# Performance work log

Hardware: AMD Instinct MI355X
Metric: run time of the kernel (lower is better)

The kernel has to match this reference:

```python
import jax, jax.numpy as jnp
import numpy as np

D_MODEL = 256
N_FEATURES = 32768
N_BLOCKS = 8
MIN_FEATURES = 512
BATCH = 2048
ALPHA = 0.99          # RunningAvgNormalizer alpha
EPS_CTRL = 3e-4       # L1RegController eps
TARGET_L0 = 100.0


def _pareto_seg(n_features, n_blocks, min_features, rng):
    # mirrors get_pareto_block_bounds, returning per-feature block ids
    cdf = 1.0 - (np.arange(n_features - min_features + 1) / (n_features - min_features + 1)) ** 0.5
    pdf = np.concatenate([np.zeros(min_features), np.abs(cdf[1:] - cdf[:-1])])
    pdf = pdf / pdf.sum()
    sp = np.sort(rng.choice(n_features, size=n_blocks - 1, replace=False, p=pdf))
    return np.searchsorted(sp, np.arange(n_features), side='right').astype(np.int32)


def setup_inputs() -> dict:
    key = jax.random.key(0)
    k0, k1 = jax.random.split(key, 2)
    x = jax.random.normal(k0, (BATCH, D_MODEL), jnp.float32)
    W_enc = jax.random.normal(k1, (D_MODEL, N_FEATURES), jnp.float32) / np.sqrt(D_MODEL)
    b_enc = -0.04 * jnp.ones((N_FEATURES,), jnp.float32)
    W_dec = (0.1 * W_enc / jnp.linalg.norm(W_enc, axis=0, keepdims=True)).T
    b_dec = jnp.zeros((D_MODEL,), jnp.float32)
    bw = np.arange(1, N_BLOCKS + 1, dtype=np.float32) ** 1.0  # block_weight_power = 1.0
    block_weights = jnp.asarray(bw / bw.max())
    running_avg = jnp.asarray([np.sqrt(D_MODEL)], jnp.float32)  # warmed-up running norm
    l1_scale = jnp.ones((1,), jnp.float32)
    seg = jnp.asarray(_pareto_seg(N_FEATURES, N_BLOCKS, MIN_FEATURES, np.random.default_rng(0)))
    return {"x": x, "W_enc": W_enc, "b_enc": b_enc, "W_dec": W_dec, "b_dec": b_dec,
            "block_weights": block_weights, "running_avg": running_avg,
            "l1_scale": l1_scale, "seg": seg}


def reference(x, W_enc, b_enc, W_dec, b_dec, block_weights, running_avg, l1_scale, seg):
    K = block_weights.shape[0]
    B, d = x.shape
    # RunningAvgNormalizer.normalize(update=True): update EMA, then scale (no grad through EMA)
    ra = ALPHA * running_avg[0] + (1.0 - ALPHA) * jnp.mean(jnp.linalg.norm(x, axis=-1))
    ra = jax.lax.stop_gradient(ra)
    xn = x * (jnp.sqrt(jnp.float32(d)) / ra)
    acts = jax.nn.relu(xn @ W_enc + b_enc)                       # [B, F]
    Wd_norms = jnp.linalg.norm(W_dec, axis=1)                    # [F]
    # per-block log-loss: sum over block features of mean-over-batch log term
    per_feat = jnp.mean(jnp.log(acts * Wd_norms + 0.1) - jnp.log(0.1), axis=0)  # [F]
    block_l1 = jax.ops.segment_sum(per_feat, seg, num_segments=K)               # [K]
    l1_loss = jnp.mean(block_weights * jnp.cumsum(block_l1))
    # per-block decode: (acts masked to block) @ W_dec, sequential over K small blocks
    onehot = (seg[None, :] == jnp.arange(K)[:, None]).astype(acts.dtype)  # [K, F]
    block_preds = jax.lax.map(lambda m: (acts * m) @ W_dec, onehot)       # [K, B, d]
    cum_preds = jnp.cumsum(block_preds, axis=0) + b_dec                   # b_dec added to preds[0] pre-cumsum
    block_errs = jnp.mean(jnp.sum((cum_preds - xn[None]) ** 2, axis=-1), axis=-1) * block_weights
    mse_loss = jnp.mean(block_errs)
    # L1RegController (no-grad)
    avg_l0 = jax.lax.stop_gradient(jnp.sum(acts > 0).astype(jnp.float32) / B)
    l1_reg_scale = jnp.where(avg_l0 < TARGET_L0, l1_scale[0] * (1.0 - EPS_CTRL), l1_scale[0] * (1.0 + EPS_CTRL))
    loss = mse_loss + l1_reg_scale * l1_loss
    return loss
```

## Files before the change

### kernel.cpp

```cpp
#include <hip/hip_runtime.h>
#include <hip/hip_fp8.h>

typedef float  f32x4  __attribute__((ext_vector_type(4)));
typedef unsigned short u16;
typedef unsigned int   u32;
typedef unsigned long long u64;

#define BATCH 2048
#define DM    256
#define NFEAT 32768
#define NBLK  8
#define ALPHA_C   0.99f
#define EPS_CTRL  3e-4f
#define TARGET_L0 100.0f

#define BT    32
#define FC    2048
#define NCHUNK (NFEAT / FC)
#define MACRO 128
#define NMACRO (FC / MACRO)
#define NPMAX 24
#define ACTS_SZ (BT * MACRO)

#define SCL_WE 8.0f
#define INV_WE 0.125f
#define SCL_WD 16.0f
#define INV_WD 0.0625f

#define WS_RA    0
#define WS_SCALE 1
#define WS_L0    2
#define WS_L1    4
#define WS_ERR   16
#define WSI_BND  32
#define WSI_PTN  40
#define WSI_PTS  41
#define WSI_PSEG 66
#define WS_WDN   256
#define PIECES_OFF_BYTES ((size_t)262144)
#define PIECES_BYTES ((size_t)NPMAX * BATCH * DM * 2)
#define WEP_OFF_BYTES (PIECES_OFF_BYTES + PIECES_BYTES)
#define WDP_OFF_BYTES (WEP_OFF_BYTES + (size_t)NFEAT * DM)

#define RAW_BARRIER() asm volatile("s_waitcnt lgkmcnt(0)\n\ts_barrier" ::: "memory")

static __device__ inline u16 f2b(float f) {
    return __builtin_bit_cast(u16, (__bf16)f);
}
static __device__ inline float b2f(u16 u) {
    return (float)__builtin_bit_cast(__bf16, u);
}
static __device__ inline u32 f2f8x2(float a, float b) {
#if __has_builtin(__builtin_amdgcn_cvt_pk_fp8_f32)
    return ((u32)__builtin_amdgcn_cvt_pk_fp8_f32(a, b, 0, false)) & 0xFFFFu;
#else
    __hip_fp8_e4m3 ha(a), hb(b);
    return (u32)(*reinterpret_cast<unsigned char*>(&ha)) |
           ((u32)(*reinterpret_cast<unsigned char*>(&hb)) << 8);
#endif
}
static __device__ inline f32x4 mfma8(u64 a, u64 b, f32x4 c) {
    return __builtin_amdgcn_mfma_f32_16x16x32_fp8_fp8((long)a, (long)b, c, 0, 0, 0);
}

__global__ __launch_bounds__(256) void k_prep(const float* __restrict__ x,
                                              const int* __restrict__ seg,
                                              float* ws) {
    const int bid = blockIdx.x;
    const int wave = threadIdx.x >> 6, lane = threadIdx.x & 63;
    if (bid < BATCH / 4) {
        const int row = bid * 4 + wave;
        const float4 v = *reinterpret_cast<const float4*>(x + (size_t)row * DM + lane * 4);
        float s = v.x * v.x + v.y * v.y + v.z * v.z + v.w * v.w;
        #pragma unroll
        for (int o = 32; o; o >>= 1) s += __shfl_xor(s, o);
        if (lane == 0) atomicAdd(&ws[WS_RA], sqrtf(s));
    } else {
        const int f = (bid - BATCH / 4) * 256 + threadIdx.x;
        if (f > 0 && f < NFEAT) {
            const int s = seg[f];
            if (s != seg[f - 1]) ((int*)ws)[WSI_BND + s] = f;
        }
    }
}

__global__ void k_pt2(const int* __restrict__ seg,
                      const float* __restrict__ ravg, float* ws) {
    __shared__ int stv[NCHUNK + NBLK];
    __shared__ int outL[NPMAX];
    __shared__ int NL;
    int* wsi = (int*)ws;
    const int t = threadIdx.x;
    if (t < NCHUNK) stv[t] = t * FC;
    else if (t < NCHUNK + NBLK - 1) stv[t] = wsi[WSI_BND + (t - NCHUNK + 1)];
    __syncthreads();
    if (t == 0) {
        int i = 0, j = NCHUNK, N = 0;
        while (i < NCHUNK || j < NCHUNK + NBLK - 1) {
            int v;
            if (i < NCHUNK && (j >= NCHUNK + NBLK - 1 || stv[i] <= stv[j])) v = stv[i++];
            else v = stv[j++];
            if (N == 0 || outL[N - 1] != v) outL[N++] = v;
        }
        NL = N;
    }
    __syncthreads();
    const int N = NL;
    if (t < N) {
        wsi[WSI_PTS + t] = outL[t];
        wsi[WSI_PSEG + t] = seg[outL[t]];
    }
    if (t == 0) {
        wsi[WSI_PTN] = N;
        wsi[WSI_PTS + N] = NFEAT;
        float ra = ALPHA_C * ravg[0] + (1.0f - ALPHA_C) * (ws[WS_RA] / (float)BATCH);
        ws[WS_SCALE] = 16.0f / ra;
    }
}

__global__ __launch_bounds__(256) void k_pack(const float* __restrict__ We,
                                              const float* __restrict__ Wd,
                                              unsigned char* __restrict__ WeP,
                                              unsigned char* __restrict__ WdP,
                                              float* ws) {
    __shared__ float tile[32][261];
    const int t = threadIdx.x;
    const int bid = blockIdx.x;
    if (bid < 1024) {
        const int kf = bid & 7, fblk = bid >> 3;
        const int f0 = fblk * 256;
        #pragma unroll
        for (int p = 0; p < 8; ++p) {
            const int r = p * 4 + (t >> 6);
            const int c = (t & 63) * 4;
            const float4 v = *reinterpret_cast<const float4*>(We + (size_t)(kf * 32 + r) * NFEAT + f0 + c);
            tile[r][c] = v.x; tile[r][c + 1] = v.y; tile[r][c + 2] = v.z; tile[r][c + 3] = v.w;
        }
        __syncthreads();
        #pragma unroll
        for (int p = 0; p < 4; ++p) {
            const int item = p * 256 + t;
            const int g = item >> 6, l = item & 63;
            const int F = fblk * 16 + g;
            float tv[8];
            #pragma unroll
            for (int i = 0; i < 8; ++i)
                tv[i] = tile[(l >> 4) * 8 + i][g * 16 + (l & 15)] * SCL_WE;
            const u32 lo = f2f8x2(tv[0], tv[1]) | (f2f8x2(tv[2], tv[3]) << 16);
            const u32 hi = f2f8x2(tv[4], tv[5]) | (f2f8x2(tv[6], tv[7]) << 16);
            *reinterpret_cast<u64*>(WeP + ((size_t)(F * 8 + kf) * 64 + l) * 8) = (u64)lo | ((u64)hi << 32);
        }
    } else {
        const int G = bid - 1024;
        #pragma unroll
        for (int p = 0; p < 8; ++p) {
            const int r = p * 4 + (t >> 6);
            const int c = (t & 63) * 4;
            const float4 v = *reinterpret_cast<const float4*>(Wd + (size_t)(G * 32 + r) * DM + c);
            tile[r][c] = v.x; tile[r][c + 1] = v.y; tile[r][c + 2] = v.z; tile[r][c + 3] = v.w;
        }
        __syncthreads();
        {
            const int row = t >> 3, part = t & 7;
            float s = 0.0f;
            #pragma unroll
            for (int j = 0; j < 32; ++j) {
                const float xv = tile[row][part * 32 + j];
                s += xv * xv;
            }
            s += __shfl_xor(s, 1); s += __shfl_xor(s, 2); s += __shfl_xor(s, 4);
            if (part == 0) ws[WS_WDN + G * 32 + row] = sqrtf(s);
        }
        #pragma unroll
        for (int p = 0; p < 4; ++p) {
            const int item = p * 256 + t;
            const int g = item >> 6, l = item & 63;
            float tv[8];
            #pragma unroll
            for (int i = 0; i < 8; ++i)
                tv[i] = tile[(l >> 4) * 8 + i][g * 16 + (l & 15)] * SCL_WD;
            const u32 lo = f2f8x2(tv[0], tv[1]) | (f2f8x2(tv[2], tv[3]) << 16);
            const u32 hi = f2f8x2(tv[4], tv[5]) | (f2f8x2(tv[6], tv[7]) << 16);
            *reinterpret_cast<u64*>(WdP + ((size_t)(g * 1024 + G) * 64 + l) * 8) = (u64)lo | ((u64)hi << 32);
        }
    }
}

__global__ __launch_bounds__(256, 2) void k_main(const float* __restrict__ x,
                                                 const float* __restrict__ be,
                                                 const int* __restrict__ seg,
                                                 float* __restrict__ ws,
                                                 u16* __restrict__ pieces,
                                                 const unsigned char* __restrict__ WeP,
                                                 const unsigned char* __restrict__ WdP) {
    __shared__ __align__(16) unsigned char xs[BT * DM];
    __shared__ __align__(16) unsigned char acts[2 * ACTS_SZ];
    __shared__ int segL[FC];
    __shared__ float lds_l1[NBLK];
    __shared__ unsigned lds_l0;
    __shared__ int s2s[NBLK];
    __shared__ int msegL[NMACRO];
    __shared__ int muniL[NMACRO];

    const int t = threadIdx.x;
    const int w = t >> 6;
    const int l = t & 63;
    const int l15 = l & 15, lg = l >> 4;
    const int f0 = blockIdx.x * FC;
    const int b0 = blockIdx.y * BT;
    const float scale = ws[WS_SCALE];
    const int* wsi = (const int*)ws;

    if (t < NBLK) lds_l1[t] = 0.0f;
    if (t == 0) lds_l0 = 0u;
    if (t < NPMAX) {
        const int N = wsi[WSI_PTN];
        if (t < N) {
            const int ps = wsi[WSI_PTS + t];
            if (ps >= f0 && ps < f0 + FC) s2s[wsi[WSI_PSEG + t]] = t;
        }
    }

    #pragma unroll
    for (int p = 0; p < 2; ++p)
        reinterpret_cast<int4*>(segL)[t + p * 256] =
            reinterpret_cast<const int4*>(seg + f0)[t + p * 256];

    #pragma unroll
    for (int p = 0; p < 8; ++p) {
        const int row = p * 4 + (t >> 6);
        const int col = (t & 63) * 4;
        const float4 v = *reinterpret_cast<const float4*>(x + (size_t)(b0 + row) * DM + col);
        const u32 w01 = f2f8x2(v.x * scale, v.y * scale);
        const u32 w23 = f2f8x2(v.z * scale, v.w * scale);
        const int e = (((row >> 4) * 8 + (col >> 5)) * 512 + ((col >> 3) & 3) * 128 + (row & 15) * 8 + (col & 7));
        *reinterpret_cast<u32*>(&xs[e]) = w01 | (w23 << 16);
    }
    __syncthreads();
    if (t < NMACRO) {
        msegL[t] = segL[t * MACRO];
        muniL[t] = (segL[t * MACRO] == segL[t * MACRO + MACRO - 1]);
    }
    __syncthreads();

    f32x4 pacc[2][4];
    #pragma unroll
    for (int i = 0; i < 2; ++i)
        #pragma unroll
        for (int j = 0; j < 4; ++j) pacc[i][j] = (f32x4)0.0f;

    int cur = msegL[0];
    float l1a0 = 0.0f, l1a1 = 0.0f;
    int myseg = -1;
    unsigned l0c = 0u;
    const int Dg0 = 4 * w;

    auto flush = [&](int s) {
        u16* pb = pieces + (size_t)s2s[s] * (BATCH * DM);
        #pragma unroll
        for (int rt = 0; rt < 2; ++rt)
            #pragma unroll
            for (int ct = 0; ct < 4; ++ct)
                #pragma unroll
                for (int r = 0; r < 4; ++r) {
                    const int row = b0 + 16 * rt + lg * 4 + r;
                    const int col = 64 * w + 16 * ct + l15;
                    pb[(size_t)row * DM + col] = f2b(pacc[rt][ct][r] * INV_WD);
                    pacc[rt][ct][r] = 0.0f;
                }
    };

    auto encodeR = [&](f32x4 (&eacc)[2][2], u64 (&we)[2][8]) {
        #pragma unroll
        for (int kf = 0; kf < 8; ++kf) {
            u64 a[2];
            #pragma unroll
            for (int rt = 0; rt < 2; ++rt)
                a[rt] = *reinterpret_cast<const u64*>(&xs[((rt * 8 + kf) * 64 + l) * 8]);
            #pragma unroll
            for (int rt = 0; rt < 2; ++rt)
                #pragma unroll
                for (int ct = 0; ct < 2; ++ct)
                    eacc[rt][ct] = mfma8(a[rt], we[ct][kf], eacc[rt][ct]);
        }
    };

    auto epilogue = [&](int it, f32x4 (&eacc)[2][2], const float* biasv, const float* wdnv) {
        const bool uni = (muniL[it] != 0);
        unsigned char* ab = acts + (it & 1) * ACTS_SZ;
        const int fbl = it * MACRO;
        #pragma unroll
        for (int ct = 0; ct < 2; ++ct) {
            const int s = uni ? msegL[it] : segL[fbl + 32 * w + 16 * ct + l15];
            if (s != myseg) {
                if (myseg >= 0) atomicAdd(&lds_l1[myseg], l1a0 + l1a1);
                l1a0 = 0.0f; l1a1 = 0.0f; myseg = s;
            }
            #pragma unroll
            for (int rt = 0; rt < 2; ++rt) {
                float av[4];
                #pragma unroll
                for (int r = 0; r < 4; ++r) {
                    float a = fmaf(eacc[rt][ct][r], INV_WE, biasv[ct]);
                    a = fmaxf(a, 0.0f);
                    l0c += (unsigned)__popcll(__ballot(a > 0.0f));
                    if (rt == 0) l1a0 += __logf(fmaf(a, wdnv[ct], 1.0f));
                    else         l1a1 += __logf(fmaf(a, wdnv[ct], 1.0f));
                    av[r] = a;
                }
                const u32 p01 = f2f8x2(av[0], av[1]);
                const u32 p23 = f2f8x2(av[2], av[3]);
                const int e0 = (rt * 4 + w) * 512 + (2 * ct + (l15 >> 3)) * 128 + (lg * 4) * 8 + (l15 & 7);
                ab[e0]      = (unsigned char)(p01 & 0xFF);
                ab[e0 + 8]  = (unsigned char)((p01 >> 8) & 0xFF);
                ab[e0 + 16] = (unsigned char)(p23 & 0xFF);
                ab[e0 + 24] = (unsigned char)((p23 >> 8) & 0xFF);
            }
        }
    };

    auto decodeR = [&](int ms, u64 (&wdv)[4][4]) {
        const unsigned char* ab = acts + (ms & 1) * ACTS_SZ;
        if (muniL[ms]) {
            const int s = msegL[ms];
            if (s != cur) { flush(cur); cur = s; }
            #pragma unroll
            for (int kf = 0; kf < 4; ++kf) {
                u64 a[2];
                #pragma unroll
                for (int rt = 0; rt < 2; ++rt)
                    a[rt] = *reinterpret_cast<const u64*>(&ab[((rt * 4 + kf) * 64 + l) * 8]);
                #pragma unroll
                for (int rt = 0; rt < 2; ++rt)
                    #pragma unroll
                    for (int ct = 0; ct < 4; ++ct)
                        pacc[rt][ct] = mfma8(a[rt], wdv[ct][kf], pacc[rt][ct]);
            }
        } else {
            const int fbl = ms * MACRO;
            #pragma unroll
            for (int kf = 0; kf < 4; ++kf) {
                const int W0 = fbl + kf * 32;
                const int s0 = segL[W0], s1 = segL[W0 + 31];
                if (s0 == s1) {
                    if (s0 != cur) { flush(cur); cur = s0; }
                    u64 a[2];
                    #pragma unroll
                    for (int rt = 0; rt < 2; ++rt)
                        a[rt] = *reinterpret_cast<const u64*>(&ab[((rt * 4 + kf) * 64 + l) * 8]);
                    #pragma unroll
                    for (int rt = 0; rt < 2; ++rt)
                        #pragma unroll
                        for (int ct = 0; ct < 4; ++ct)
                            pacc[rt][ct] = mfma8(a[rt], wdv[ct][kf], pacc[rt][ct]);
                } else {
                    int lo = 0;
                    while (lo < 32) {
                        const int s = segL[W0 + lo];
                        int hi = lo + 1;
                        while (hi < 32 && segL[W0 + hi] == s) ++hi;
                        if (s != cur) { flush(cur); cur = s; }
                        const int loB = min(max(lo - lg * 8, 0), 8);
                        const int hiB = min(max(hi - lg * 8, 0), 8);
                        const int n = hiB - loB;
                        u64 mask = 0;
                        if (n >= 8) mask = ~0ull;
                        else if (n > 0) mask = ((1ull << (n * 8)) - 1ull) << (loB * 8);
                        #pragma unroll
                        for (int rt = 0; rt < 2; ++rt) {
                            const u64 a = (*reinterpret_cast<const u64*>(&ab[((rt * 4 + kf) * 64 + l) * 8])) & mask;
                            #pragma unroll
                            for (int ct = 0; ct < 4; ++ct)
                                pacc[rt][ct] = mfma8(a, wdv[ct][kf], pacc[rt][ct]);
                        }
                        lo = hi;
                    }
                }
            }
        }
    };

    {
        u64 we[2][8];
        const int F0 = (f0 >> 4) + 2 * w;
        #pragma unroll
        for (int kf = 0; kf < 8; ++kf)
            #pragma unroll
            for (int ct = 0; ct < 2; ++ct)
                we[ct][kf] = *reinterpret_cast<const u64*>(WeP + (((size_t)(F0 + ct) * 8 + kf) * 64 + l) * 8);
        float biasv[2], wdnv[2];
        #pragma unroll
        for (int ct = 0; ct < 2; ++ct) {
            const int fg = f0 + 32 * w + 16 * ct + l15;
            biasv[ct] = be[fg];
            wdnv[ct] = ws[WS_WDN + fg] * 10.0f;
        }
        f32x4 eacc[2][2];
        #pragma unroll
        for (int i = 0; i < 2; ++i)
            #pragma unroll
            for (int j = 0; j < 2; ++j) eacc[i][j] = (f32x4)0.0f;
        encodeR(eacc, we);
        epilogue(0, eacc, biasv, wdnv);
    }

    for (int it = 1; it <= NMACRO; ++it) {
        RAW_BARRIER();
        const int itm1 = it - 1;

        if (it < NMACRO) {
            u64 we[2][8];
            const int F0 = ((f0 + it * MACRO) >> 4) + 2 * w;
            #pragma unroll
            for (int kf = 0; kf < 8; ++kf)
                #pragma unroll
                for (int ct = 0; ct < 2; ++ct)
                    we[ct][kf] = *reinterpret_cast<const u64*>(WeP + (((size_t)(F0 + ct) * 8 + kf) * 64 + l) * 8);
            u64 wdv[4][4];
            const int G0 = (f0 + itm1 * MACRO) >> 5;
            #pragma unroll
            for (int kf = 0; kf < 4; ++kf)
                #pragma unroll
                for (int ct = 0; ct < 4; ++ct)
                    wdv[ct][kf] = *reinterpret_cast<const u64*>(WdP + (((size_t)(Dg0 + ct) * 1024 + G0 + kf) * 64 + l) * 8);
            float biasv[2], wdnv[2];
            #pragma unroll
            for (int ct = 0; ct < 2; ++ct) {
                const int fg = f0 + it * MACRO + 32 * w + 16 * ct + l15;
                biasv[ct] = be[fg];
                wdnv[ct] = ws[WS_WDN + fg] * 10.0f;
            }

            f32x4 eacc[2][2];
            #pragma unroll
            for (int i = 0; i < 2; ++i)
                #pragma unroll
                for (int j = 0; j < 2; ++j) eacc[i][j] = (f32x4)0.0f;
            encodeR(eacc, we);
            decodeR(itm1, wdv);
            epilogue(it, eacc, biasv, wdnv);
        } else {
            u64 wdv[4][4];
            const int G0 = (f0 + itm1 * MACRO) >> 5;
            #pragma unroll
            for (int kf = 0; kf < 4; ++kf)
                #pragma unroll
                for (int ct = 0; ct < 4; ++ct)
                    wdv[ct][kf] = *reinterpret_cast<const u64*>(WdP + (((size_t)(Dg0 + ct) * 1024 + G0 + kf) * 64 + l) * 8);
            decodeR(itm1, wdv);
        }
    }

    flush(cur);
    if (myseg >= 0) atomicAdd(&lds_l1[myseg], l1a0 + l1a1);
    if (l == 0) atomicAdd(&lds_l0, l0c);
    __syncthreads();
    if (t < NBLK) atomicAdd(&ws[WS_L1 + t], lds_l1[t]);
    if (t == 0) atomicAdd(((unsigned*)ws) + WS_L0, lds_l0);
}


__global__ __launch_bounds__(256) void k_err(const float* __restrict__ x,
                                             const float* __restrict__ bd,
                                             float* ws,
                                             const u16* __restrict__ pieces) {
    const int b = blockIdx.x, t = threadIdx.x;
    const int wave = t >> 6, lane = t & 63;
    const int* wsi = (const int*)ws;
    const int N = wsi[WSI_PTN];
    const float scale = ws[WS_SCALE];
    const float xv = x[(size_t)b * DM + t] * scale;
    float p = bd[t];
    __shared__ float lds[NBLK][4];
    for (int i = 0; i < N; ++i) {
        p += b2f(pieces[(size_t)i * (BATCH * DM) + (size_t)b * DM + t]);
        const int sg = wsi[WSI_PSEG + i];
        const bool end = (i == N - 1) || (wsi[WSI_PSEG + i + 1] != sg);
        if (end) {
            const float d = p - xv;
            float e = d * d;
            #pragma unroll
            for (int o = 32; o; o >>= 1) e += __shfl_xor(e, o);
            if (lane == 0) lds[sg][wave] = e;
        }
    }
    __syncthreads();
    if (t < NBLK) {
        const float s = lds[t][0] + lds[t][1] + lds[t][2] + lds[t][3];
        atomicAdd(&ws[WS_ERR + t], s);
    }
}

__global__ void k_loss(const float* __restrict__ bw,
                       const float* __restrict__ l1s,
                       const float* ws, float* out) {
    float cum = 0.0f, l1 = 0.0f, mse = 0.0f;
    for (int k = 0; k < NBLK; ++k) {
        cum += ws[WS_L1 + k] / (float)BATCH;
        l1 += bw[k] * cum;
        mse += bw[k] * (ws[WS_ERR + k] / (float)BATCH);
    }
    l1 *= (1.0f / NBLK);
    mse *= (1.0f / NBLK);
    const unsigned l0 = ((const unsigned*)ws)[WS_L0];
    const float avg_l0 = (float)l0 / (float)BATCH;
    const float rs = l1s[0] * (avg_l0 < TARGET_L0 ? (1.0f - EPS_CTRL) : (1.0f + EPS_CTRL));
    out[0] = mse + rs * l1;
}


extern "C" void kernel_launch(void* const* d_in, const int* in_sizes, int n_in,
                              void* d_out, int out_size, void* d_ws, size_t ws_size,
                              hipStream_t stream) {
    const float* x    = (const float*)d_in[0];
    const float* We   = (const float*)d_in[1];
    const float* be   = (const float*)d_in[2];
    const float* Wd   = (const float*)d_in[3];
    const float* bd   = (const float*)d_in[4];
    const float* bw   = (const float*)d_in[5];
    const float* ravg = (const float*)d_in[6];
    const float* l1s  = (const float*)d_in[7];
    const int*   seg  = (const int*)d_in[8];
    float* out = (float*)d_out;
    float* ws  = (float*)d_ws;
    u16* pieces = (u16*)((char*)d_ws + PIECES_OFF_BYTES);
    unsigned char* WeP = (unsigned char*)d_ws + WEP_OFF_BYTES;
    unsigned char* WdP = (unsigned char*)d_ws + WDP_OFF_BYTES;

    hipMemsetAsync(d_ws, 0, 1024, stream);
    k_prep<<<BATCH / 4 + NFEAT / 256, 256, 0, stream>>>(x, seg, ws);
    k_pack<<<2048, 256, 0, stream>>>(We, Wd, WeP, WdP, ws);
    k_pt2<<<1, 64, 0, stream>>>(seg, ravg, ws);
    dim3 g(NFEAT / FC, BATCH / BT);
    k_main<<<g, 256, 0, stream>>>(x, be, seg, ws, pieces, WeP, WdP);
    k_err<<<BATCH, 256, 0, stream>>>(x, bd, ws, pieces);
    k_loss<<<1, 1, 0, stream>>>(bw, l1s, ws, out);
}
```

Before: 212.1 us.

## Software-pipeline weight prefetch one macro-step ahead and use per-lane L0 counts

```diff
diff --git a/kernel.cpp b/kernel.cpp
--- a/kernel.cpp
+++ b/kernel.cpp
@@ -303,7 +303,7 @@
                 for (int r = 0; r < 4; ++r) {
                     float a = fmaf(eacc[rt][ct][r], INV_WE, biasv[ct]);
                     a = fmaxf(a, 0.0f);
-                    l0c += (unsigned)__popcll(__ballot(a > 0.0f));
+                    l0c += (a > 0.0f) ? 1u : 0u;
                     if (rt == 0) l1a0 += __logf(fmaf(a, wdnv[ct], 1.0f));
                     else         l1a1 += __logf(fmaf(a, wdnv[ct], 1.0f));
                     av[r] = a;
@@ -380,80 +380,75 @@
         }
     };
 
+    u64 we[2][8];
+    u64 wdv[4][4];
+    float biasC[2], wdnC[2];
+
     {
-        u64 we[2][8];
         const int F0 = (f0 >> 4) + 2 * w;
         #pragma unroll
         for (int kf = 0; kf < 8; ++kf)
             #pragma unroll
             for (int ct = 0; ct < 2; ++ct)
                 we[ct][kf] = *reinterpret_cast<const u64*>(WeP + (((size_t)(F0 + ct) * 8 + kf) * 64 + l) * 8);
-        float biasv[2], wdnv[2];
         #pragma unroll
         for (int ct = 0; ct < 2; ++ct) {
             const int fg = f0 + 32 * w + 16 * ct + l15;
-            biasv[ct] = be[fg];
-            wdnv[ct] = ws[WS_WDN + fg] * 10.0f;
-        }
+            biasC[ct] = be[fg];
+            wdnC[ct] = ws[WS_WDN + fg] * 10.0f;
+        }
+    }
+
+    for (int it = 0; it < NMACRO; ++it) {
+        if (it > 0) RAW_BARRIER();
+
         f32x4 eacc[2][2];
         #pragma unroll
         for (int i = 0; i < 2; ++i)
             #pragma unroll
             for (int j = 0; j < 2; ++j) eacc[i][j] = (f32x4)0.0f;
+
         encodeR(eacc, we);
-        epilogue(0, eacc, biasv, wdnv);
-    }
-
-    for (int it = 1; it <= NMACRO; ++it) {
-        RAW_BARRIER();
-        const int itm1 = it - 1;
-
-        if (it < NMACRO) {
-            u64 we[2][8];
-            const int F0 = ((f0 + it * MACRO) >> 4) + 2 * w;
+        if (it > 0) decodeR(it - 1, wdv);
+
+        float biasN[2], wdnN[2];
+        if (it + 1 < NMACRO) {
+            const int F0 = ((f0 + (it + 1) * MACRO) >> 4) + 2 * w;
             #pragma unroll
             for (int kf = 0; kf < 8; ++kf)
                 #pragma unroll
                 for (int ct = 0; ct < 2; ++ct)
                     we[ct][kf] = *reinterpret_cast<const u64*>(WeP + (((size_t)(F0 + ct) * 8 + kf) * 64 + l) * 8);
-            u64 wdv[4][4];
-            const int G0 = (f0 + itm1 * MACRO) >> 5;
+            #pragma unroll
+            for (int ct = 0; ct < 2; ++ct) {
+                const int fg = f0 + (it + 1) * MACRO + 32 * w + 16 * ct + l15;
+                biasN[ct] = be[fg];
+                wdnN[ct] = ws[WS_WDN + fg] * 10.0f;
+            }
+        } else {
+            biasN[0] = biasN[1] = 0.0f;
+            wdnN[0] = wdnN[1] = 0.0f;
+        }
+        {
+            const int G0 = (f0 + it * MACRO) >> 5;
             #pragma unroll
             for (int kf = 0; kf < 4; ++kf)
                 #pragma unroll
                 for (int ct = 0; ct < 4; ++ct)
                     wdv[ct][kf] = *reinterpret_cast<const u64*>(WdP + (((size_t)(Dg0 + ct) * 1024 + G0 + kf) * 64 + l) * 8);
-            float biasv[2], wdnv[2];
-            #pragma unroll
-            for (int ct = 0; ct < 2; ++ct) {
-                const int fg = f0 + it * MACRO + 32 * w + 16 * ct + l15;
-                biasv[ct] = be[fg];
-                wdnv[ct] = ws[WS_WDN + fg] * 10.0f;
-            }
-
-            f32x4 eacc[2][2];
-            #pragma unroll
-            for (int i = 0; i < 2; ++i)
-                #pragma unroll
-                for (int j = 0; j < 2; ++j) eacc[i][j] = (f32x4)0.0f;
-            encodeR(eacc, we);
-            decodeR(itm1, wdv);
-            epilogue(it, eacc, biasv, wdnv);
-        } else {
-            u64 wdv[4][4];
-            const int G0 = (f0 + itm1 * MACRO) >> 5;
-            #pragma unroll
-            for (int kf = 0; kf < 4; ++kf)
-                #pragma unroll
-                for (int ct = 0; ct < 4; ++ct)
-                    wdv[ct][kf] = *reinterpret_cast<const u64*>(WdP + (((size_t)(Dg0 + ct) * 1024 + G0 + kf) * 64 + l) * 8);
-            decodeR(itm1, wdv);
-        }
-    }
+        }
+
+        epilogue(it, eacc, biasC, wdnC);
+        biasC[0] = biasN[0]; biasC[1] = biasN[1];
+        wdnC[0] = wdnN[0];  wdnC[1] = wdnN[1];
+    }
+
+    RAW_BARRIER();
+    decodeR(NMACRO - 1, wdv);
 
     flush(cur);
     if (myseg >= 0) atomicAdd(&lds_l1[myseg], l1a0 + l1a1);
-    if (l == 0) atomicAdd(&lds_l0, l0c);
+    atomicAdd(&lds_l0, l0c);
     __syncthreads();
     if (t < NBLK) atomicAdd(&ws[WS_L1 + t], lds_l1[t]);
     if (t == 0) atomicAdd(((unsigned*)ws) + WS_L0, lds_l0);
```

After: 224.7 us. 5.9% more time.
